# Optimization experiments

Measured on AMD Instinct MI355X. Metric: run time of the kernel, lower is better.

Reference implementation:

```python
import jax, jax.numpy as jnp
import numpy as np

B, S, E, H = 4, 2048, 1024, 16
D = E // H  # head_dim = 64

def setup_inputs() -> dict:
    key = jax.random.key(0)
    k1, k2, k3 = jax.random.split(key, 3)
    x = jax.random.normal(k1, (B, S, E), dtype=jnp.float32)
    # nn.Linear(E, 3E, bias=False): y = x @ W^T; we store W already transposed as [E, 3E]
    w_qkv = jax.random.normal(k2, (E, 3 * E), dtype=jnp.float32) * (E ** -0.5)
    w_out = jax.random.normal(k3, (E, E), dtype=jnp.float32) * (E ** -0.5)
    b_out = jnp.zeros((E,), dtype=jnp.float32)
    return {"x": x, "w_qkv": w_qkv, "w_out": w_out, "b_out": b_out}

def reference(x, w_qkv, w_out, b_out):
    b, s, e = x.shape
    h, d = H, e // H
    # qkv projection then rearrange 'b s (qkv h d) -> qkv b h s d'
    qkv = (x @ w_qkv).reshape(b, s, 3, h, d).transpose(2, 0, 3, 1, 4)
    q, k, v = qkv[0], qkv[1], qkv[2]            # each [b, h, s, d]
    scale = jnp.asarray(d, x.dtype) ** -0.5
    att = jnp.einsum('bhxd,bhyd->bhxy', q, k) * scale   # [b, h, s, s]
    att = jax.nn.softmax(att, axis=-1)
    o = jnp.einsum('bhxy,bhyd->bhxd', att, v)           # [b, h, s, d]
    o = o.transpose(0, 2, 1, 3).reshape(b, s, e)        # 'b h s d -> b s (h d)'
    return o @ w_out + b_out
```

## Files before the change

kernel.cpp:

```cpp
#include <hip/hip_runtime.h>
#include <cstdint>
#include <cstddef>


typedef __attribute__((ext_vector_type(8))) short short8;
typedef __attribute__((ext_vector_type(4))) float float4_;
typedef unsigned int u32;
typedef unsigned short u16;

__device__ __forceinline__ u16 f2b(float f) {
  u32 u = __float_as_uint(f);
  u += 0x7FFFu + ((u >> 16) & 1u);
  return (u16)(u >> 16);
}

__device__ __forceinline__ float fexp2(float x) {
#if __has_builtin(__builtin_amdgcn_exp2f)
  return __builtin_amdgcn_exp2f(x);
#else
  return exp2f(x);
#endif
}

__device__ __forceinline__ u32 pk_trunc(float lo, float hi) {
#if __has_builtin(__builtin_amdgcn_perm)
  return __builtin_amdgcn_perm(__float_as_uint(hi), __float_as_uint(lo), 0x07060302);
#else
  return (__float_as_uint(hi) & 0xFFFF0000u) | (__float_as_uint(lo) >> 16);
#endif
}

#if __has_builtin(__builtin_amdgcn_fdot2_f32_bf16)
typedef __bf16 bf16x2 __attribute__((ext_vector_type(2)));
__device__ __forceinline__ float accum_pk(u32 pk, float acc) {
  bf16x2 p = __builtin_bit_cast(bf16x2, pk);
  bf16x2 one = __builtin_bit_cast(bf16x2, (u32)0x3F803F80u);
  return __builtin_amdgcn_fdot2_f32_bf16(p, one, acc, false);
}
#else
__device__ __forceinline__ float accum_pk(u32 pk, float acc) {
  return acc + __uint_as_float(pk << 16) + __uint_as_float(pk & 0xFFFF0000u);
}
#endif

__device__ __forceinline__ void async_cp16(const void* g, void* l) {
  __builtin_amdgcn_global_load_lds(
      (const __attribute__((address_space(1))) u32*)g,
      (__attribute__((address_space(3))) u32*)l, 16, 0, 0);
}


__device__ __forceinline__ void transpose_block(const float* __restrict__ in,
                                                u16* __restrict__ out,
                                                int R, int C, int bx, int by,
                                                float t[32][33]) {
  int tx = threadIdx.x & 31, ty = threadIdx.x >> 5;
  int r0 = by * 32, c0 = bx * 32;
#pragma unroll
  for (int k = 0; k < 4; k++)
    t[ty + 8 * k][tx] = in[(size_t)(r0 + ty + 8 * k) * C + c0 + tx];
  __syncthreads();
#pragma unroll
  for (int k = 0; k < 4; k++)
    out[(size_t)(c0 + ty + 8 * k) * R + r0 + tx] = f2b(t[tx][ty + 8 * k]);
}

__global__ void prepass_kernel(const float* __restrict__ x, u16* __restrict__ Xb,
                               const float* __restrict__ wqkv, u16* __restrict__ Wqt,
                               const float* __restrict__ wout, u16* __restrict__ Wot) {
  __shared__ float t[32][33];
  int gid = blockIdx.x;
  if (gid < 8192) {
    int i = gid * 256 + threadIdx.x;
    float4 v = ((const float4*)x)[i];
    uint2 p;
    p.x = (u32)f2b(v.x) | ((u32)f2b(v.y) << 16);
    p.y = (u32)f2b(v.z) | ((u32)f2b(v.w) << 16);
    ((uint2*)Xb)[i] = p;
  } else if (gid < 11264) {
    int j = gid - 8192;
    transpose_block(wqkv, Wqt, 1024, 3072, j % 96, j / 96, t);
  } else {
    int j = gid - 11264;
    transpose_block(wout, Wot, 1024, 1024, j % 32, j / 32, t);
  }
}

__global__ void transpose_v(const u16* __restrict__ V, u16* __restrict__ Vt) {
  __shared__ u16 t[64][80];
  int bh = blockIdx.y, s0 = blockIdx.x * 64;
  const u16* Vh = V + (size_t)bh * 2048 * 64;
  u16* Vth = Vt + (size_t)bh * 64 * 2048;
  int tr = threadIdx.x >> 3;
  int tc = (threadIdx.x & 7) * 8;
#pragma unroll
  for (int p = 0; p < 2; p++) {
    int r = p * 32 + tr;
    *(uint4*)&t[r][tc] = *(const uint4*)(Vh + (size_t)(s0 + r) * 64 + tc);
  }
  __syncthreads();
#pragma unroll
  for (int p = 0; p < 2; p++) {
    int d = p * 32 + tr;
    u16 tmp[8];
#pragma unroll
    for (int k = 0; k < 8; k++) tmp[k] = t[tc + k][d];
    *(uint4*)(Vth + (size_t)d * 2048 + s0 + tc) = *(uint4*)tmp;
  }
}


__global__ __launch_bounds__(256) void gemm_qkv_kernel(
    const u16* __restrict__ A, const u16* __restrict__ Bt,
    u16* __restrict__ QKV) {
  const int K = 1024;
  __shared__ short8 lA[2][512];
  __shared__ short8 lB[2][512];
  int tid = threadIdx.x;
  int w = tid >> 6, l = tid & 63, lr = l & 15, lq = l >> 4;
  int gid = blockIdx.x;
  int xcd = gid & 7, j = gid >> 3;
  int yloc = j & 7, xt = j >> 3;
  int m0 = (xcd * 8 + yloc) * 128, n0 = xt * 128;
  int wm = w & 1, wn = w >> 1;
  float4_ acc[4][4] = {};

  const u16* gA0 = A + (size_t)(m0 + w * 32 + lr) * K + lq * 8;
  const u16* gA1 = gA0 + 16 * K;
  const u16* gB0 = Bt + (size_t)(n0 + w * 32 + lr) * K + lq * 8;
  const u16* gB1 = gB0 + 16 * K;

  auto stage = [&](int buf, int k0) {
    async_cp16(gA0 + k0, &lA[buf][(w * 2 + 0) * 64 + l]);
    async_cp16(gA1 + k0, &lA[buf][(w * 2 + 1) * 64 + l]);
    async_cp16(gB0 + k0, &lB[buf][(w * 2 + 0) * 64 + l]);
    async_cp16(gB1 + k0, &lB[buf][(w * 2 + 1) * 64 + l]);
  };
  auto compute = [&](int buf) {
    short8 af[4], bf[4];
#pragma unroll
    for (int t = 0; t < 4; t++) {
      af[t] = lA[buf][(wm * 4 + t) * 64 + l];
      bf[t] = lB[buf][(wn * 4 + t) * 64 + l];
    }
#pragma unroll
    for (int mt = 0; mt < 4; mt++)
#pragma unroll
      for (int nt = 0; nt < 4; nt++)
        acc[mt][nt] = __builtin_amdgcn_mfma_f32_16x16x32_bf16(af[mt], bf[nt], acc[mt][nt], 0, 0, 0);
  };

  stage(0, 0);
  for (int k0 = 0; k0 < K; k0 += 64) {
    __syncthreads();
    stage(1, k0 + 32);
    compute(0);
    __syncthreads();
    if (k0 + 64 < K) stage(0, k0 + 64);
    compute(1);
  }

  const float qsc = 0.18033688011112042f;
#pragma unroll
  for (int nt = 0; nt < 4; nt++) {
    int gn = n0 + wn * 64 + nt * 16 + lr;
    int sel = gn >> 10;
    int h = (gn >> 6) & 15;
    int d = gn & 63;
    float sc = (sel == 0) ? qsc : 1.0f;
    u16* dst = QKV + (size_t)sel * 8388608 + ((size_t)h * 2048) * 64 + d;
#pragma unroll
    for (int mt = 0; mt < 4; mt++) {
#pragma unroll
      for (int r = 0; r < 4; r++) {
        int gm = m0 + wm * 64 + mt * 16 + lq * 4 + r;
        int b = gm >> 11, s = gm & 2047;
        dst[((size_t)b * 16 * 2048 + s) * 64] = f2b(acc[mt][nt][r] * sc);
      }
    }
  }
}

__global__ __launch_bounds__(256) void gemm_out_kernel(
    const u16* __restrict__ A, const u16* __restrict__ Bt,
    const float* __restrict__ bias, float* __restrict__ out) {
  const int K = 1024;
  __shared__ short8 lA[2][512];
  __shared__ short8 lB[2][512];
  int tid = threadIdx.x;
  int w = tid >> 6, l = tid & 63, lr = l & 15, lq = l >> 4;
  int gid = blockIdx.x;
  int xcd = gid & 7, j = gid >> 3;
  int yloc = j & 7, xt = j >> 3;
  int m0 = (xcd * 8 + yloc) * 128, n0 = xt * 128;
  int wm = w & 1, wn = w >> 1;
  float4_ acc[4][4] = {};

  const u16* gA0 = A + (size_t)(m0 + w * 32 + lr) * K + lq * 8;
  const u16* gA1 = gA0 + 16 * K;
  const u16* gB0 = Bt + (size_t)(n0 + w * 32 + lr) * K + lq * 8;
  const u16* gB1 = gB0 + 16 * K;

  auto stage = [&](int buf, int k0) {
    async_cp16(gA0 + k0, &lA[buf][(w * 2 + 0) * 64 + l]);
    async_cp16(gA1 + k0, &lA[buf][(w * 2 + 1) * 64 + l]);
    async_cp16(gB0 + k0, &lB[buf][(w * 2 + 0) * 64 + l]);
    async_cp16(gB1 + k0, &lB[buf][(w * 2 + 1) * 64 + l]);
  };
  auto compute = [&](int buf) {
    short8 af[4], bf[4];
#pragma unroll
    for (int t = 0; t < 4; t++) {
      af[t] = lA[buf][(wm * 4 + t) * 64 + l];
      bf[t] = lB[buf][(wn * 4 + t) * 64 + l];
    }
#pragma unroll
    for (int mt = 0; mt < 4; mt++)
#pragma unroll
      for (int nt = 0; nt < 4; nt++)
        acc[mt][nt] = __builtin_amdgcn_mfma_f32_16x16x32_bf16(af[mt], bf[nt], acc[mt][nt], 0, 0, 0);
  };

  stage(0, 0);
  for (int k0 = 0; k0 < K; k0 += 64) {
    __syncthreads();
    stage(1, k0 + 32);
    compute(0);
    __syncthreads();
    if (k0 + 64 < K) stage(0, k0 + 64);
    compute(1);
  }

#pragma unroll
  for (int nt = 0; nt < 4; nt++) {
    int gn = n0 + wn * 64 + nt * 16 + lr;
    float bv = bias[gn];
#pragma unroll
    for (int mt = 0; mt < 4; mt++)
#pragma unroll
      for (int r = 0; r < 4; r++) {
        int gm = m0 + wm * 64 + mt * 16 + lq * 4 + r;
        out[(size_t)gm * 1024 + gn] = acc[mt][nt][r] + bv;
      }
  }
}


__global__ __launch_bounds__(256) void attn_kernel(
    const u16* __restrict__ Qb, const u16* __restrict__ Kb,
    const u16* __restrict__ Vt, u16* __restrict__ Ob, int bh_base) {
  const int S = 2048, D = 64;
  __shared__ short8 lK[2][512];
  __shared__ short8 lV[2][512];
  __shared__ __align__(16) u32 pb[4][16][20];
  int tid = threadIdx.x;
  int w = tid >> 6, l = tid & 63, lr = l & 15, lq = l >> 4;
  int gid = blockIdx.x;
  int xcd = gid & 7, j = gid >> 3;
  int bh = bh_base + xcd * 4 + (j >> 4);
  int qblk = j & 15;
  int q0 = qblk * 128 + w * 32;
  const u16* Qh = Qb + (size_t)bh * S * D;
  const u16* Kh = Kb + (size_t)bh * S * D;
  const u16* Vh = Vt + (size_t)bh * D * S;

  short8 qf[2][2];
#pragma unroll
  for (int qg = 0; qg < 2; qg++) {
    qf[qg][0] = *(const short8*)(Qh + (q0 + qg * 16 + lr) * D + lq * 8);
    qf[qg][1] = *(const short8*)(Qh + (q0 + qg * 16 + lr) * D + 32 + lq * 8);
  }

  float ls[2][4] = {};
  float4_ o[2][4] = {};

  const u16* kg = Kh + (size_t)(((w >> 1) << 5) + 2 * lr + (w & 1)) * D + lq * 8;
  const u16* vg = Vh + (size_t)(w * 16 + lr) * S + lq * 8;

  auto stage = [&](int buf, int kv0) {
    async_cp16(kg + (size_t)kv0 * D, &lK[buf][(w * 2 + 0) * 64 + l]);
    async_cp16(kg + (size_t)kv0 * D + 32, &lK[buf][(w * 2 + 1) * 64 + l]);
    async_cp16(vg + kv0, &lV[buf][(w * 2 + 0) * 64 + l]);
    async_cp16(vg + kv0 + 32, &lV[buf][(w * 2 + 1) * 64 + l]);
  };

  auto compute = [&](int buf) {
#pragma unroll
    for (int sub = 0; sub < 2; sub++) {
      short8 ke0 = lK[buf][((sub * 2 + 0) * 2 + 0) * 64 + l];
      short8 ke1 = lK[buf][((sub * 2 + 0) * 2 + 1) * 64 + l];
      short8 ko0 = lK[buf][((sub * 2 + 1) * 2 + 0) * 64 + l];
      short8 ko1 = lK[buf][((sub * 2 + 1) * 2 + 1) * 64 + l];
#pragma unroll
      for (int qg = 0; qg < 2; qg++) {
        float4_ z = {0.f, 0.f, 0.f, 0.f};
        float4_ s0 = __builtin_amdgcn_mfma_f32_16x16x32_bf16(qf[qg][0], ke0, z, 0, 0, 0);
        s0 = __builtin_amdgcn_mfma_f32_16x16x32_bf16(qf[qg][1], ke1, s0, 0, 0, 0);
        float4_ s1 = __builtin_amdgcn_mfma_f32_16x16x32_bf16(qf[qg][0], ko0, z, 0, 0, 0);
        s1 = __builtin_amdgcn_mfma_f32_16x16x32_bf16(qf[qg][1], ko1, s1, 0, 0, 0);
#pragma unroll
        for (int r = 0; r < 4; r++) {
          float p0 = fexp2(s0[r]);
          float p1 = fexp2(s1[r]);
          u32 pk = pk_trunc(p0, p1);
          ls[qg][r] = accum_pk(pk, ls[qg][r]);
          pb[w][lq * 4 + r][lr] = pk;
        }
        short8 pa = *(const short8*)&pb[w][lr][lq * 4];
#pragma unroll
        for (int dt = 0; dt < 4; dt++)
          o[qg][dt] = __builtin_amdgcn_mfma_f32_16x16x32_bf16(
              pa, lV[buf][(dt * 2 + sub) * 64 + l], o[qg][dt], 0, 0, 0);
      }
    }
  };

  stage(0, 0);
  for (int kv0 = 0; kv0 < S; kv0 += 128) {
    __syncthreads();
    stage(1, kv0 + 64);
    compute(0);
    __syncthreads();
    if (kv0 + 128 < S) stage(0, kv0 + 128);
    compute(1);
  }

  int b = bh >> 4, h = bh & 15;
#pragma unroll
  for (int qg = 0; qg < 2; qg++) {
    float inv[4];
#pragma unroll
    for (int r = 0; r < 4; r++) {
      float s = ls[qg][r];
#pragma unroll
      for (int off = 1; off < 16; off <<= 1) s += __shfl_xor(s, off, 64);
      inv[r] = 1.0f / s;
    }
#pragma unroll
    for (int dt = 0; dt < 4; dt++)
#pragma unroll
      for (int r = 0; r < 4; r++) {
        int s_ = q0 + qg * 16 + lq * 4 + r;
        Ob[((size_t)(b * 2048 + s_)) * 1024 + h * 64 + dt * 16 + lr] =
            f2b(o[qg][dt][r] * inv[r]);
      }
  }
}


extern "C" void kernel_launch(void* const* d_in, const int* in_sizes, int n_in,
                              void* d_out, int out_size, void* d_ws, size_t ws_size,
                              hipStream_t stream) {
  const float* x     = (const float*)d_in[0];
  const float* w_qkv = (const float*)d_in[1];
  const float* w_out = (const float*)d_in[2];
  const float* b_out = (const float*)d_in[3];
  float* out = (float*)d_out;

  char* ws = (char*)d_ws;
  u16* Xb  = (u16*)(ws);
  u16* Wqt = (u16*)(ws + (16u << 20));
  u16* Wot = (u16*)(ws + (22u << 20));
  u16* QKV = (u16*)(ws + (24u << 20));
  u16* Qb  = QKV;
  u16* Kb  = QKV + 8388608;
  u16* Vb  = QKV + 16777216;
  u16* Vt  = (u16*)(ws + (72u << 20));
  u16* Ob  = Xb;

  prepass_kernel<<<12288, 256, 0, stream>>>(x, Xb, w_qkv, Wqt, w_out, Wot);
  gemm_qkv_kernel<<<1536, 256, 0, stream>>>(Xb, Wqt, QKV);
  transpose_v<<<dim3(32, 64), 256, 0, stream>>>(Vb, Vt);
  attn_kernel<<<512, 256, 0, stream>>>(Qb, Kb, Vt, Ob, 0);
  attn_kernel<<<512, 256, 0, stream>>>(Qb, Kb, Vt, Ob, 32);
  gemm_out_kernel<<<512, 256, 0, stream>>>(Ob, Wot, b_out, out);
}
```

Baseline: 344.2 us.

## Use 256x256 tiles with interleaved staging in QKV GEMM; merge attention launches

The QKV projection GEMM moves from 128x128 tiles with 4 waves to 256x256 tiles with 8 waves. Its K-loop is software-pipelined: global-to-LDS copies are split into quarter stages interleaved with MFMA blocks, guarded by explicit waitcnt, barriers and s_setprio. The aim is higher data reuse per tile and better overlap of loads with matrix math, at the cost of more LDS and registers and fewer blocks (384). Separately, the two attention launches are merged into one grid of 1024 blocks to remove a launch and the tail between them.

```diff
diff --git a/kernel.cpp b/kernel.cpp
--- a/kernel.cpp
+++ b/kernel.cpp
@@ -110,76 +110,148 @@
 }
 
 
-__global__ __launch_bounds__(256) void gemm_qkv_kernel(
+__global__ __launch_bounds__(512, 2) void gemm_qkv_kernel(
     const u16* __restrict__ A, const u16* __restrict__ Bt,
     u16* __restrict__ QKV) {
   const int K = 1024;
-  __shared__ short8 lA[2][512];
-  __shared__ short8 lB[2][512];
+  const int NT = 16;
+  __shared__ short8 lA[2][2048];
+  __shared__ short8 lB[2][2048];
   int tid = threadIdx.x;
-  int w = tid >> 6, l = tid & 63, lr = l & 15, lq = l >> 4;
+  int wid = tid >> 6, l = tid & 63, lr = l & 15, lq = l >> 4;
+  int wm = wid >> 2, wn = wid & 3;
   int gid = blockIdx.x;
   int xcd = gid & 7, j = gid >> 3;
-  int yloc = j & 7, xt = j >> 3;
-  int m0 = (xcd * 8 + yloc) * 128, n0 = xt * 128;
-  int wm = w & 1, wn = w >> 1;
-  float4_ acc[4][4] = {};
-
-  const u16* gA0 = A + (size_t)(m0 + w * 32 + lr) * K + lq * 8;
-  const u16* gA1 = gA0 + 16 * K;
-  const u16* gB0 = Bt + (size_t)(n0 + w * 32 + lr) * K + lq * 8;
-  const u16* gB1 = gB0 + 16 * K;
-
-  auto stage = [&](int buf, int k0) {
-    async_cp16(gA0 + k0, &lA[buf][(w * 2 + 0) * 64 + l]);
-    async_cp16(gA1 + k0, &lA[buf][(w * 2 + 1) * 64 + l]);
-    async_cp16(gB0 + k0, &lB[buf][(w * 2 + 0) * 64 + l]);
-    async_cp16(gB1 + k0, &lB[buf][(w * 2 + 1) * 64 + l]);
-  };
-  auto compute = [&](int buf) {
-    short8 af[4], bf[4];
-#pragma unroll
-    for (int t = 0; t < 4; t++) {
-      af[t] = lA[buf][(wm * 4 + t) * 64 + l];
-      bf[t] = lB[buf][(wn * 4 + t) * 64 + l];
+  int nt = j % 12, mt = xcd * 4 + j / 12;
+  int m0 = mt * 256, n0 = nt * 256;
+
+  float4_ acc[8][4] = {};
+
+  const u16* srcA[2][2];
+  const u16* srcB[2][2];
+#pragma unroll
+  for (int h = 0; h < 2; h++)
+#pragma unroll
+    for (int s = 0; s < 2; s++) {
+      int fl = h * 16 + s * 8 + (tid >> 6);
+      int fr = fl >> 1, ks = fl & 1;
+      srcA[h][s] = A + (size_t)(m0 + fr * 16 + lr) * K + ks * 32 + lq * 8;
+      srcB[h][s] = Bt + (size_t)(n0 + fr * 16 + lr) * K + ks * 32 + lq * 8;
     }
-#pragma unroll
-    for (int mt = 0; mt < 4; mt++)
-#pragma unroll
-      for (int nt = 0; nt < 4; nt++)
-        acc[mt][nt] = __builtin_amdgcn_mfma_f32_16x16x32_bf16(af[mt], bf[nt], acc[mt][nt], 0, 0, 0);
-  };
-
-  stage(0, 0);
-  for (int k0 = 0; k0 < K; k0 += 64) {
-    __syncthreads();
-    stage(1, k0 + 32);
-    compute(0);
-    __syncthreads();
-    if (k0 + 64 < K) stage(0, k0 + 64);
-    compute(1);
-  }
+
+  auto stageA = [&](int buf, int h, int k0) {
+#pragma unroll
+    for (int s = 0; s < 2; s++)
+      async_cp16(srcA[h][s] + k0, &lA[buf][h * 1024 + s * 512 + tid]);
+  };
+  auto stageB = [&](int buf, int h, int k0) {
+#pragma unroll
+    for (int s = 0; s < 2; s++)
+      async_cp16(srcB[h][s] + k0, &lB[buf][h * 1024 + s * 512 + tid]);
+  };
+
+  stageB(0, 0, 0); stageB(0, 1, 0);
+  stageA(0, 0, 0); stageA(0, 1, 0);
+  stageB(1, 0, 64); stageB(1, 1, 64);
+  asm volatile("s_waitcnt vmcnt(4)" ::: "memory");
+  __builtin_amdgcn_sched_barrier(0);
+  __builtin_amdgcn_s_barrier();
+
+  short8 areg[4], breg[4][2];
+  for (int u = 0; u < NT; ++u) {
+    int buf = u & 1, nbuf = buf ^ 1;
+    int kA = (u < NT - 1 ? u + 1 : NT - 1) * 64;
+    int kB = (u < NT - 2 ? u + 2 : NT - 1) * 64;
+
+#pragma unroll
+    for (int nf = 0; nf < 4; nf++) breg[nf][0] = lB[buf][((wn * 4 + nf) * 2 + 0) * 64 + l];
+#pragma unroll
+    for (int mf = 0; mf < 4; mf++) areg[mf] = lA[buf][((wm * 8 + mf) * 2 + 0) * 64 + l];
+    stageA(nbuf, 0, kA);
+    __builtin_amdgcn_s_barrier();
+    asm volatile("s_waitcnt lgkmcnt(0)" ::: "memory");
+    __builtin_amdgcn_sched_barrier(0);
+    __builtin_amdgcn_s_setprio(1);
+#pragma unroll
+    for (int mf = 0; mf < 4; mf++)
+#pragma unroll
+      for (int nf = 0; nf < 4; nf++)
+        acc[mf][nf] = __builtin_amdgcn_mfma_f32_16x16x32_bf16(areg[mf], breg[nf][0], acc[mf][nf], 0, 0, 0);
+    __builtin_amdgcn_s_setprio(0);
+    __builtin_amdgcn_s_barrier();
+
+#pragma unroll
+    for (int nf = 0; nf < 4; nf++) breg[nf][1] = lB[buf][((wn * 4 + nf) * 2 + 1) * 64 + l];
+#pragma unroll
+    for (int mf = 0; mf < 4; mf++) areg[mf] = lA[buf][((wm * 8 + 4 + mf) * 2 + 0) * 64 + l];
+    stageA(nbuf, 1, kA);
+    __builtin_amdgcn_s_barrier();
+    asm volatile("s_waitcnt lgkmcnt(0)" ::: "memory");
+    __builtin_amdgcn_sched_barrier(0);
+    __builtin_amdgcn_s_setprio(1);
+#pragma unroll
+    for (int mf = 0; mf < 4; mf++)
+#pragma unroll
+      for (int nf = 0; nf < 4; nf++)
+        acc[4 + mf][nf] = __builtin_amdgcn_mfma_f32_16x16x32_bf16(areg[mf], breg[nf][0], acc[4 + mf][nf], 0, 0, 0);
+    __builtin_amdgcn_s_setprio(0);
+    __builtin_amdgcn_s_barrier();
+
+#pragma unroll
+    for (int mf = 0; mf < 4; mf++) areg[mf] = lA[buf][((wm * 8 + mf) * 2 + 1) * 64 + l];
+    stageB(buf, 0, kB);
+    __builtin_amdgcn_s_barrier();
+    asm volatile("s_waitcnt lgkmcnt(0)" ::: "memory");
+    __builtin_amdgcn_sched_barrier(0);
+    __builtin_amdgcn_s_setprio(1);
+#pragma unroll
+    for (int mf = 0; mf < 4; mf++)
+#pragma unroll
+      for (int nf = 0; nf < 4; nf++)
+        acc[mf][nf] = __builtin_amdgcn_mfma_f32_16x16x32_bf16(areg[mf], breg[nf][1], acc[mf][nf], 0, 0, 0);
+    __builtin_amdgcn_s_setprio(0);
+    __builtin_amdgcn_s_barrier();
+
+#pragma unroll
+    for (int mf = 0; mf < 4; mf++) areg[mf] = lA[buf][((wm * 8 + 4 + mf) * 2 + 1) * 64 + l];
+    stageB(buf, 1, kB);
+    __builtin_amdgcn_s_barrier();
+    asm volatile("s_waitcnt lgkmcnt(0)" ::: "memory");
+    __builtin_amdgcn_sched_barrier(0);
+    __builtin_amdgcn_s_setprio(1);
+#pragma unroll
+    for (int mf = 0; mf < 4; mf++)
+#pragma unroll
+      for (int nf = 0; nf < 4; nf++)
+        acc[4 + mf][nf] = __builtin_amdgcn_mfma_f32_16x16x32_bf16(areg[mf], breg[nf][1], acc[4 + mf][nf], 0, 0, 0);
+    __builtin_amdgcn_s_setprio(0);
+    asm volatile("s_waitcnt vmcnt(4)" ::: "memory");
+    __builtin_amdgcn_sched_barrier(0);
+    __builtin_amdgcn_s_barrier();
+  }
+  asm volatile("s_waitcnt vmcnt(0)" ::: "memory");
 
   const float qsc = 0.18033688011112042f;
 #pragma unroll
-  for (int nt = 0; nt < 4; nt++) {
-    int gn = n0 + wn * 64 + nt * 16 + lr;
+  for (int nf = 0; nf < 4; nf++) {
+    int gn = n0 + wn * 64 + nf * 16 + lr;
     int sel = gn >> 10;
     int h = (gn >> 6) & 15;
     int d = gn & 63;
     float sc = (sel == 0) ? qsc : 1.0f;
     u16* dst = QKV + (size_t)sel * 8388608 + ((size_t)h * 2048) * 64 + d;
 #pragma unroll
-    for (int mt = 0; mt < 4; mt++) {
+    for (int mf = 0; mf < 8; mf++) {
 #pragma unroll
       for (int r = 0; r < 4; r++) {
-        int gm = m0 + wm * 64 + mt * 16 + lq * 4 + r;
+        int gm = m0 + wm * 128 + mf * 16 + lq * 4 + r;
         int b = gm >> 11, s = gm & 2047;
-        dst[((size_t)b * 16 * 2048 + s) * 64] = f2b(acc[mt][nt][r] * sc);
+        dst[((size_t)b * 16 * 2048 + s) * 64] = f2b(acc[mf][nf][r] * sc);
       }
     }
   }
 }
+
 
 __global__ __launch_bounds__(256) void gemm_out_kernel(
     const u16* __restrict__ A, const u16* __restrict__ Bt,
@@ -248,7 +320,7 @@
 
 __global__ __launch_bounds__(256) void attn_kernel(
     const u16* __restrict__ Qb, const u16* __restrict__ Kb,
-    const u16* __restrict__ Vt, u16* __restrict__ Ob, int bh_base) {
+    const u16* __restrict__ Vt, u16* __restrict__ Ob) {
   const int S = 2048, D = 64;
   __shared__ short8 lK[2][512];
   __shared__ short8 lV[2][512];
@@ -257,7 +329,7 @@
   int w = tid >> 6, l = tid & 63, lr = l & 15, lq = l >> 4;
   int gid = blockIdx.x;
   int xcd = gid & 7, j = gid >> 3;
-  int bh = bh_base + xcd * 4 + (j >> 4);
+  int bh = xcd * 8 + (j >> 4);
   int qblk = j & 15;
   int q0 = qblk * 128 + w * 32;
   const u16* Qh = Qb + (size_t)bh * S * D;
@@ -369,9 +441,8 @@
   u16* Ob  = Xb;
 
   prepass_kernel<<<12288, 256, 0, stream>>>(x, Xb, w_qkv, Wqt, w_out, Wot);
-  gemm_qkv_kernel<<<1536, 256, 0, stream>>>(Xb, Wqt, QKV);
+  gemm_qkv_kernel<<<384, 512, 0, stream>>>(Xb, Wqt, QKV);
   transpose_v<<<dim3(32, 64), 256, 0, stream>>>(Vb, Vt);
-  attn_kernel<<<512, 256, 0, stream>>>(Qb, Kb, Vt, Ob, 0);
-  attn_kernel<<<512, 256, 0, stream>>>(Qb, Kb, Vt, Ob, 32);
+  attn_kernel<<<1024, 256, 0, stream>>>(Qb, Kb, Vt, Ob);
   gemm_out_kernel<<<512, 256, 0, stream>>>(Ob, Wot, b_out, out);
 }
```

New measurement: 338.1 us. Within noise of the previous version (-1.8%).

## Compute transposed scores to keep P in registers; merge attention launches

Applied to the files above, without the earlier changes.

Swaps the MFMA operand order so the score tile comes out transposed (kv along the row dimension). It also reorders how K rows are staged into LDS so each lane's exponentiated scores already line up with the PV MFMA's A operand, using two cross-half shuffles instead of a per-warp LDS round trip. Row sums are now kept as one scalar per lane and reduced once at the end. The two half-grid attention launches become a single 1024-block launch. This removes LDS traffic and the wait on P in the inner loop plus one launch, at the cost of a more intricate K permutation and extra lane shuffles.

```diff
diff --git a/kernel.cpp b/kernel.cpp
--- a/kernel.cpp
+++ b/kernel.cpp
@@ -5,6 +5,7 @@
 
 typedef __attribute__((ext_vector_type(8))) short short8;
 typedef __attribute__((ext_vector_type(4))) float float4_;
+typedef __attribute__((ext_vector_type(4))) unsigned int u32x4;
 typedef unsigned int u32;
 typedef unsigned short u16;
 
@@ -248,16 +249,15 @@
 
 __global__ __launch_bounds__(256) void attn_kernel(
     const u16* __restrict__ Qb, const u16* __restrict__ Kb,
-    const u16* __restrict__ Vt, u16* __restrict__ Ob, int bh_base) {
+    const u16* __restrict__ Vt, u16* __restrict__ Ob) {
   const int S = 2048, D = 64;
   __shared__ short8 lK[2][512];
   __shared__ short8 lV[2][512];
-  __shared__ __align__(16) u32 pb[4][16][20];
   int tid = threadIdx.x;
   int w = tid >> 6, l = tid & 63, lr = l & 15, lq = l >> 4;
   int gid = blockIdx.x;
   int xcd = gid & 7, j = gid >> 3;
-  int bh = bh_base + xcd * 4 + (j >> 4);
+  int bh = xcd * 8 + (j >> 4);
   int qblk = j & 15;
   int q0 = qblk * 128 + w * 32;
   const u16* Qh = Qb + (size_t)bh * S * D;
@@ -271,15 +271,23 @@
     qf[qg][1] = *(const short8*)(Qh + (q0 + qg * 16 + lr) * D + 32 + lq * 8);
   }
 
-  float ls[2][4] = {};
+  float ls[2] = {};
   float4_ o[2][4] = {};
 
-  const u16* kg = Kh + (size_t)(((w >> 1) << 5) + 2 * lr + (w & 1)) * D + lq * 8;
+  const u16* kgsrc[2];
+#pragma unroll
+  for (int i = 0; i < 2; i++) {
+    int f = (w & 1) * 2 + i;
+    int sub = w >> 1;
+    int kvl = sub * 32 + ((f < 2) ? (8 * (lr >> 2) + (lr & 3))
+                                  : (8 * ((lr >> 2) ^ 2) + 4 + (lr & 3)));
+    kgsrc[i] = Kh + (size_t)kvl * D + (f & 1) * 32 + lq * 8;
+  }
   const u16* vg = Vh + (size_t)(w * 16 + lr) * S + lq * 8;
 
   auto stage = [&](int buf, int kv0) {
-    async_cp16(kg + (size_t)kv0 * D, &lK[buf][(w * 2 + 0) * 64 + l]);
-    async_cp16(kg + (size_t)kv0 * D + 32, &lK[buf][(w * 2 + 1) * 64 + l]);
+    async_cp16(kgsrc[0] + (size_t)kv0 * D, &lK[buf][(w * 2 + 0) * 64 + l]);
+    async_cp16(kgsrc[1] + (size_t)kv0 * D, &lK[buf][(w * 2 + 1) * 64 + l]);
     async_cp16(vg + kv0, &lV[buf][(w * 2 + 0) * 64 + l]);
     async_cp16(vg + kv0 + 32, &lV[buf][(w * 2 + 1) * 64 + l]);
   };
@@ -287,26 +295,31 @@
   auto compute = [&](int buf) {
 #pragma unroll
     for (int sub = 0; sub < 2; sub++) {
-      short8 ke0 = lK[buf][((sub * 2 + 0) * 2 + 0) * 64 + l];
-      short8 ke1 = lK[buf][((sub * 2 + 0) * 2 + 1) * 64 + l];
-      short8 ko0 = lK[buf][((sub * 2 + 1) * 2 + 0) * 64 + l];
-      short8 ko1 = lK[buf][((sub * 2 + 1) * 2 + 1) * 64 + l];
+      short8 kf0 = lK[buf][(sub * 4 + 0) * 64 + l];
+      short8 kf1 = lK[buf][(sub * 4 + 1) * 64 + l];
+      short8 kf2 = lK[buf][(sub * 4 + 2) * 64 + l];
+      short8 kf3 = lK[buf][(sub * 4 + 3) * 64 + l];
 #pragma unroll
       for (int qg = 0; qg < 2; qg++) {
         float4_ z = {0.f, 0.f, 0.f, 0.f};
-        float4_ s0 = __builtin_amdgcn_mfma_f32_16x16x32_bf16(qf[qg][0], ke0, z, 0, 0, 0);
-        s0 = __builtin_amdgcn_mfma_f32_16x16x32_bf16(qf[qg][1], ke1, s0, 0, 0, 0);
-        float4_ s1 = __builtin_amdgcn_mfma_f32_16x16x32_bf16(qf[qg][0], ko0, z, 0, 0, 0);
-        s1 = __builtin_amdgcn_mfma_f32_16x16x32_bf16(qf[qg][1], ko1, s1, 0, 0, 0);
-#pragma unroll
-        for (int r = 0; r < 4; r++) {
-          float p0 = fexp2(s0[r]);
-          float p1 = fexp2(s1[r]);
-          u32 pk = pk_trunc(p0, p1);
-          ls[qg][r] = accum_pk(pk, ls[qg][r]);
-          pb[w][lq * 4 + r][lr] = pk;
-        }
-        short8 pa = *(const short8*)&pb[w][lr][lq * 4];
+        float4_ s0 = __builtin_amdgcn_mfma_f32_16x16x32_bf16(kf0, qf[qg][0], z, 0, 0, 0);
+        s0 = __builtin_amdgcn_mfma_f32_16x16x32_bf16(kf1, qf[qg][1], s0, 0, 0, 0);
+        float4_ s1 = __builtin_amdgcn_mfma_f32_16x16x32_bf16(kf2, qf[qg][0], z, 0, 0, 0);
+        s1 = __builtin_amdgcn_mfma_f32_16x16x32_bf16(kf3, qf[qg][1], s1, 0, 0, 0);
+        float p00 = fexp2(s0[0]), p01 = fexp2(s0[1]);
+        float p02 = fexp2(s0[2]), p03 = fexp2(s0[3]);
+        float p10 = fexp2(s1[0]), p11 = fexp2(s1[1]);
+        float p12 = fexp2(s1[2]), p13 = fexp2(s1[3]);
+        u32 w0 = pk_trunc(p00, p01), w1 = pk_trunc(p02, p03);
+        u32 y0 = pk_trunc(p10, p11), y1 = pk_trunc(p12, p13);
+        float a = ls[qg];
+        a = accum_pk(w0, a); a = accum_pk(w1, a);
+        a = accum_pk(y0, a); a = accum_pk(y1, a);
+        ls[qg] = a;
+        u32 W2 = (u32)__shfl_xor((int)y0, 32, 64);
+        u32 W3 = (u32)__shfl_xor((int)y1, 32, 64);
+        u32x4 pw = {w0, w1, W2, W3};
+        short8 pa = __builtin_bit_cast(short8, pw);
 #pragma unroll
         for (int dt = 0; dt < 4; dt++)
           o[qg][dt] = __builtin_amdgcn_mfma_f32_16x16x32_bf16(
@@ -328,14 +341,13 @@
   int b = bh >> 4, h = bh & 15;
 #pragma unroll
   for (int qg = 0; qg < 2; qg++) {
+    float s = ls[qg];
+    s += __shfl_xor(s, 16, 64);
+    s += __shfl_xor(s, 32, 64);
     float inv[4];
 #pragma unroll
-    for (int r = 0; r < 4; r++) {
-      float s = ls[qg][r];
-#pragma unroll
-      for (int off = 1; off < 16; off <<= 1) s += __shfl_xor(s, off, 64);
-      inv[r] = 1.0f / s;
-    }
+    for (int r = 0; r < 4; r++)
+      inv[r] = 1.0f / __shfl(s, lq * 4 + r, 64);
 #pragma unroll
     for (int dt = 0; dt < 4; dt++)
 #pragma unroll
@@ -371,7 +383,6 @@
   prepass_kernel<<<12288, 256, 0, stream>>>(x, Xb, w_qkv, Wqt, w_out, Wot);
   gemm_qkv_kernel<<<1536, 256, 0, stream>>>(Xb, Wqt, QKV);
   transpose_v<<<dim3(32, 64), 256, 0, stream>>>(Vb, Vt);
-  attn_kernel<<<512, 256, 0, stream>>>(Qb, Kb, Vt, Ob, 0);
-  attn_kernel<<<512, 256, 0, stream>>>(Qb, Kb, Vt, Ob, 32);
+  attn_kernel<<<1024, 256, 0, stream>>>(Qb, Kb, Vt, Ob);
   gemm_out_kernel<<<512, 256, 0, stream>>>(Ob, Wot, b_out, out);
 }
```

Measured after the change: 337.3 us. -2.0%, faster.
